# Kernel optimization log

Measured on AMD Instinct MI355X. Metric: run time of the kernel, lower is better.

## Reference

```python
import jax, jax.numpy as jnp
import numpy as np

B, C, E, H = 8, 2048, 1024, 128


def setup_inputs() -> dict:
    key = jax.random.key(0)
    k1, k2, k3, k4 = jax.random.split(key, 4)
    x = jax.random.normal(k1, (B, C, E), dtype=jnp.float32)
    # store projection weights as (E, H) so projection is x @ W
    Wq = jax.random.normal(k2, (E, H), dtype=jnp.float32) * (E ** -0.5)
    Wk = jax.random.normal(k3, (E, H), dtype=jnp.float32) * (E ** -0.5)
    Wv = jax.random.normal(k4, (E, H), dtype=jnp.float32) * (E ** -0.5)
    return {"x": x, "Wq": Wq, "Wk": Wk, "Wv": Wv}


def reference(x, Wq, Wk, Wv):
    # x: (B, C, E) -> out: (B, C, H)
    _, c, e = x.shape
    q = x @ Wq  # (B, C, H)
    k = x @ Wk  # (B, C, H)
    v = x @ Wv  # (B, C, H)
    # NOTE: original scales by embed_size**0.5, not head_size**0.5
    scale = jnp.asarray(e, x.dtype) ** 0.5
    w = jnp.einsum('bqh,bkh->bqk', q, k) / scale  # (B, C, C)
    causal = jnp.tril(jnp.ones((c, c), dtype=bool))
    w = jnp.where(causal, w, -jnp.inf)
    w = jax.nn.softmax(w, axis=-1)
    # dropout_rate = 0.0 -> identity (eval mode)
    out = w @ v  # (B, C, H)
    return out
```

## Files before the change

kernel.cpp:

```cpp
#include <hip/hip_runtime.h>
#include <hip/hip_bf16.h>
#include <stdint.h>

#define B_ 8
#define C_ 2048
#define E_ 1024
#define H_ 128
#define M_ (B_*C_)
#define SLOTS_B 144

typedef __attribute__((ext_vector_type(8))) short bf16x8;
typedef __attribute__((ext_vector_type(4))) float f32x4;

__device__ __forceinline__ unsigned short f2bf(float f) {
    union { float f; unsigned int u; } v; v.f = f;
    unsigned int u = v.u;
    u += 0x7fff + ((u >> 16) & 1);
    return (unsigned short)(u >> 16);
}
__device__ __forceinline__ float bf2f(unsigned short u) {
    union { unsigned int i; float f; } v; v.i = ((unsigned int)u) << 16; return v.f;
}

#define GLOAD_LDS16(g, l) \
    __builtin_amdgcn_global_load_lds((const __attribute__((address_space(1))) void*)(g), \
                                     (__attribute__((address_space(3))) void*)(l), 16, 0, 0)

__global__ __launch_bounds__(256) void wt2_kernel(const float* __restrict__ Wq,
                                                  const float* __restrict__ Wk,
                                                  const float* __restrict__ Wv,
                                                  unsigned short* __restrict__ WT2) {
    int z = blockIdx.y;
    const float* W = (z == 0) ? Wq : (z == 1) ? Wk : Wv;
    unsigned short* o = WT2 + (size_t)z * H_ * E_;
    int gid = blockIdx.x * 256 + threadIdx.x;
    int g = gid >> 7, h = gid & 127;
    unsigned short t[8];
#pragma unroll
    for (int j = 0; j < 8; ++j)
        t[j] = f2bf(W[(size_t)(g * 8 + j) * H_ + h]);
    *(bf16x8*)&o[(size_t)(g * 128 + h) * 8] = *(const bf16x8*)t;
}

#define MF(a, b, c) __builtin_amdgcn_mfma_f32_16x16x32_bf16((a), (b), (c), 0, 0, 0)

#define ALOAD(S, T) { const float* xs_ = xrow + (T) * 64; \
    a##S##_0 = *(const float4*)xs_;        a##S##_1 = *(const float4*)(xs_ + 4); \
    a##S##_2 = *(const float4*)(xs_ + 8);  a##S##_3 = *(const float4*)(xs_ + 12); }

#define AWRITE(S, BUF) { \
    unsigned short t0_[8] = {f2bf(a##S##_0.x), f2bf(a##S##_0.y), f2bf(a##S##_0.z), f2bf(a##S##_0.w), \
                             f2bf(a##S##_1.x), f2bf(a##S##_1.y), f2bf(a##S##_1.z), f2bf(a##S##_1.w)}; \
    unsigned short t1_[8] = {f2bf(a##S##_2.x), f2bf(a##S##_2.y), f2bf(a##S##_2.z), f2bf(a##S##_2.w), \
                             f2bf(a##S##_3.x), f2bf(a##S##_3.y), f2bf(a##S##_3.z), f2bf(a##S##_3.w)}; \
    *(bf16x8*)&As[BUF][arow][(ag0 ^ (arow & 7)) * 8]       = *(const bf16x8*)t0_; \
    *(bf16x8*)&As[BUF][arow][((ag0 + 1) ^ (arow & 7)) * 8] = *(const bf16x8*)t1_; }

#define BLOAD(S, T) { const unsigned short* wp_ = wbase + (size_t)(T) * 8192; \
    b##S##0 = *(const bf16x8*)(wp_);        b##S##1 = *(const bf16x8*)(wp_ + 128); \
    b##S##2 = *(const bf16x8*)(wp_ + 256);  b##S##3 = *(const bf16x8*)(wp_ + 384); \
    b##S##4 = *(const bf16x8*)(wp_ + 4096); b##S##5 = *(const bf16x8*)(wp_ + 4224); \
    b##S##6 = *(const bf16x8*)(wp_ + 4352); b##S##7 = *(const bf16x8*)(wp_ + 4480); }

#define COMPUTE(BUF, S) { \
    bf16x8 af00 = *(const bf16x8*)&As[BUF][ra0][(lq ^ (ra0 & 7)) * 8]; \
    bf16x8 af01 = *(const bf16x8*)&As[BUF][ra1][(lq ^ (ra1 & 7)) * 8]; \
    acc[0][0] = MF(af00, b##S##0, acc[0][0]);  acc[1][0] = MF(af01, b##S##0, acc[1][0]); \
    acc[0][1] = MF(af00, b##S##1, acc[0][1]);  acc[1][1] = MF(af01, b##S##1, acc[1][1]); \
    acc[0][2] = MF(af00, b##S##2, acc[0][2]);  acc[1][2] = MF(af01, b##S##2, acc[1][2]); \
    acc[0][3] = MF(af00, b##S##3, acc[0][3]);  acc[1][3] = MF(af01, b##S##3, acc[1][3]); \
    bf16x8 af10 = *(const bf16x8*)&As[BUF][ra0][((4 + lq) ^ (ra0 & 7)) * 8]; \
    bf16x8 af11 = *(const bf16x8*)&As[BUF][ra1][((4 + lq) ^ (ra1 & 7)) * 8]; \
    acc[0][0] = MF(af10, b##S##4, acc[0][0]);  acc[1][0] = MF(af11, b##S##4, acc[1][0]); \
    acc[0][1] = MF(af10, b##S##5, acc[0][1]);  acc[1][1] = MF(af11, b##S##5, acc[1][1]); \
    acc[0][2] = MF(af10, b##S##6, acc[0][2]);  acc[1][2] = MF(af11, b##S##6, acc[1][2]); \
    acc[0][3] = MF(af10, b##S##7, acc[0][3]);  acc[1][3] = MF(af11, b##S##7, acc[1][3]); }

#define EVEN_STEP(K) { \
    __syncthreads(); \
    AWRITE(B, 1);                                   \
    if ((K) + 3 <= 15) ALOAD(B, (K) + 3); \
    COMPUTE(0, A);                                  \
    if ((K) + 2 <= 15) BLOAD(A, (K) + 2); }

#define ODD_STEP(K) { \
    __syncthreads(); \
    if ((K) + 1 <= 15) AWRITE(A, 0);                \
    if ((K) + 3 <= 15) ALOAD(A, (K) + 3); \
    COMPUTE(1, B);                                  \
    if ((K) + 2 <= 15) BLOAD(B, (K) + 2); }

__global__ __launch_bounds__(256) void proj_kernel(const float* __restrict__ x,
                                                   const unsigned short* __restrict__ WT2,
                                                   unsigned short* __restrict__ QKV) {
    __shared__ __align__(16) unsigned short As[2][64][64];

    const int tid = threadIdx.x;
    const int wid = tid >> 6, lane = tid & 63;
    const int lrow = lane & 15, lq = lane >> 4;
    const int wr = wid >> 1, wc = wid & 1;
    const int row0 = blockIdx.x * 64;
    const int w = blockIdx.y;
    const unsigned short* wt = WT2 + (size_t)w * H_ * E_;

    const int arow = tid >> 2;
    const int ag0 = (tid & 3) * 2;
    const float* xrow = x + (size_t)(row0 + arow) * E_ + ag0 * 8;
    const int ra0 = wr * 32 + lrow, ra1 = wr * 32 + 16 + lrow;

    const unsigned short* wbase = wt + (size_t)(lq * 128 + wc * 64 + lrow) * 8;

    f32x4 acc[2][4];
#pragma unroll
    for (int mi = 0; mi < 2; ++mi)
#pragma unroll
        for (int ni = 0; ni < 4; ++ni) acc[mi][ni] = (f32x4){0.f, 0.f, 0.f, 0.f};

    float4 aA_0, aA_1, aA_2, aA_3, aB_0, aB_1, aB_2, aB_3;
    bf16x8 bA0, bA1, bA2, bA3, bA4, bA5, bA6, bA7;
    bf16x8 bB0, bB1, bB2, bB3, bB4, bB5, bB6, bB7;

    ALOAD(A, 0); BLOAD(A, 0);
    ALOAD(B, 1); BLOAD(B, 1);
    AWRITE(A, 0);
    ALOAD(A, 2);

    EVEN_STEP(0)  ODD_STEP(1)  EVEN_STEP(2)  ODD_STEP(3)
    EVEN_STEP(4)  ODD_STEP(5)  EVEN_STEP(6)  ODD_STEP(7)
    EVEN_STEP(8)  ODD_STEP(9)  EVEN_STEP(10) ODD_STEP(11)
    EVEN_STEP(12) ODD_STEP(13) EVEN_STEP(14) ODD_STEP(15)

    if (w < 2) {
        const float qs = (w == 0) ? 0.03125f : 1.0f;
        unsigned short* outp = QKV + (size_t)w * M_ * H_;
#pragma unroll
        for (int mi = 0; mi < 2; ++mi) {
            int r0 = row0 + wr * 32 + mi * 16 + lq * 4;
#pragma unroll
            for (int ni = 0; ni < 4; ++ni) {
                int col = wc * 64 + ni * 16 + lrow;
#pragma unroll
                for (int r = 0; r < 4; ++r)
                    outp[(size_t)(r0 + r) * H_ + col] = f2bf(acc[mi][ni][r] * qs);
            }
        }
    } else {
        unsigned short* vt = QKV + (size_t)2 * M_ * H_;
        int b = row0 / C_;
        int cbase = row0 % C_;
#pragma unroll
        for (int mi = 0; mi < 2; ++mi) {
            int c0 = cbase + wr * 32 + mi * 16 + lq * 4;
#pragma unroll
            for (int ni = 0; ni < 4; ++ni) {
                int h = wc * 64 + ni * 16 + lrow;
                __align__(8) unsigned short p[4] = {f2bf(acc[mi][ni][0]), f2bf(acc[mi][ni][1]),
                                                    f2bf(acc[mi][ni][2]), f2bf(acc[mi][ni][3])};
                *(uint2*)&vt[((size_t)b * H_ + h) * C_ + c0] = *(const uint2*)p;
            }
        }
    }
}

__global__ __launch_bounds__(256) void attn_kernel(const unsigned short* __restrict__ QKV,
                                                   unsigned short* __restrict__ PO,
                                                   float* __restrict__ ML,
                                                   float* __restrict__ out) {
    __shared__ __align__(16) unsigned short Ks[2][64][128];
    __shared__ __align__(16) unsigned short Vt[2][128][64];
    __shared__ __align__(16) unsigned short Ps[4][16][72];

    const unsigned short* Q  = QKV;
    const unsigned short* K  = QKV + (size_t)M_ * H_;
    const unsigned short* VT = QKV + (size_t)2 * M_ * H_;

    const int tid = threadIdx.x, wid = tid >> 6, lane = tid & 63;
    const int lrow = lane & 15, lq = lane >> 4, lk = lq * 8;
    const int rr = blockIdx.x;
    const int b = blockIdx.y;

    int j = 0;
#pragma unroll
    for (int jj = 1; jj < 32; ++jj) {
        int q = jj >> 2, s = jj & 3;
        if (jj + 2 * q * (q - 1) + s * q <= rr) j = jj;
    }
    const int qj = j >> 2, sj = j & 3;
    const int Cj = j + 2 * qj * (qj - 1) + sj * qj;
    const int c = rr - Cj;
    const int nch = qj + 1;
    const int t0 = c * 4;
    const int t1 = min(t0 + 4, j + 1);

    const int q0w = j * 64 + wid * 16;
    const unsigned short* Kb  = K  + (size_t)b * C_ * H_;
    const unsigned short* VTb = VT + (size_t)b * H_ * C_;
    const int qrow0 = q0w + lq * 4;

    const int krow = tid >> 4, kg = tid & 15;
    const int vrow = tid >> 3, vg = tid & 7;

    bf16x8 qf[4];
#pragma unroll
    for (int kf = 0; kf < 4; ++kf)
        qf[kf] = *(const bf16x8*)&Q[((size_t)b * C_ + q0w + lrow) * H_ + kf * 32 + lk];

    f32x4 o[8];
#pragma unroll
    for (int nf = 0; nf < 8; ++nf) o[nf] = (f32x4){0.f, 0.f, 0.f, 0.f};
    float m[4] = {-INFINITY, -INFINITY, -INFINITY, -INFINITY};
    float l[4] = {0.f, 0.f, 0.f, 0.f};

    auto STAGE = [&](int buf, int t) {
        const int kv0 = t * 64;
#pragma unroll
        for (int s = 0; s < 4; ++s) {
            int r = s * 16 + krow;
            GLOAD_LDS16(&Kb[(size_t)(kv0 + r) * H_ + ((kg ^ (r & 15)) * 8)],
                        (char*)&Ks[buf][0][0] + s * 4096 + tid * 16);
        }
#pragma unroll
        for (int s = 0; s < 4; ++s) {
            int h = s * 32 + vrow;
            GLOAD_LDS16(&VTb[(size_t)h * C_ + kv0 + ((vg ^ (h & 7)) * 8)],
                        (char*)&Vt[buf][0][0] + s * 4096 + tid * 16);
        }
    };

    STAGE(0, t0);

    for (int t = t0; t < t1; ++t) {
        const int cur = (t - t0) & 1;
        __syncthreads();
        if (t + 1 < t1) STAGE(cur ^ 1, t + 1);

        const int kv0 = t * 64;
        f32x4 s[4];
#pragma unroll
        for (int nf = 0; nf < 4; ++nf) {
            s[nf] = (f32x4){0.f, 0.f, 0.f, 0.f};
            const int rk = nf * 16 + lrow;
#pragma unroll
            for (int kf = 0; kf < 4; ++kf) {
                bf16x8 kb = *(const bf16x8*)&Ks[cur][rk][((kf * 4 + lq) ^ (rk & 15)) * 8];
                s[nf] = __builtin_amdgcn_mfma_f32_16x16x32_bf16(qf[kf], kb, s[nf], 0, 0, 0);
            }
        }
        bf16x8 vb[8][2];
#pragma unroll
        for (int nf = 0; nf < 8; ++nf) {
            const int h = nf * 16 + lrow;
#pragma unroll
            for (int kf2 = 0; kf2 < 2; ++kf2)
                vb[nf][kf2] = *(const bf16x8*)&Vt[cur][h][((kf2 * 4 + lq) ^ (h & 7)) * 8];
        }

        if (t == j) {
#pragma unroll
            for (int nf = 0; nf < 4; ++nf) {
                int key = kv0 + nf * 16 + lrow;
#pragma unroll
                for (int r = 0; r < 4; ++r)
                    if (key > qrow0 + r) s[nf][r] = -INFINITY;
            }
        }
        float mt[4] = {-INFINITY, -INFINITY, -INFINITY, -INFINITY};
#pragma unroll
        for (int nf = 0; nf < 4; ++nf)
#pragma unroll
            for (int r = 0; r < 4; ++r) mt[r] = fmaxf(mt[r], s[nf][r]);
#pragma unroll
        for (int r = 0; r < 4; ++r)
#pragma unroll
            for (int off = 1; off < 16; off <<= 1)
                mt[r] = fmaxf(mt[r], __shfl_xor(mt[r], off));

        float corr[4];
#pragma unroll
        for (int r = 0; r < 4; ++r) {
            float mn = fmaxf(m[r], mt[r]);
            corr[r] = __expf(m[r] - mn);
            m[r] = mn;
        }
        float ps[4] = {0.f, 0.f, 0.f, 0.f};
#pragma unroll
        for (int nf = 0; nf < 4; ++nf)
#pragma unroll
            for (int r = 0; r < 4; ++r) {
                float p = __expf(s[nf][r] - m[r]);
                ps[r] += p;
                Ps[wid][lq * 4 + r][nf * 16 + lrow] = f2bf(p);
            }
#pragma unroll
        for (int r = 0; r < 4; ++r) {
#pragma unroll
            for (int off = 1; off < 16; off <<= 1) ps[r] += __shfl_xor(ps[r], off);
            l[r] = l[r] * corr[r] + ps[r];
        }
#pragma unroll
        for (int nf = 0; nf < 8; ++nf)
#pragma unroll
            for (int r = 0; r < 4; ++r) o[nf][r] *= corr[r];

        bf16x8 pa[2];
#pragma unroll
        for (int kf2 = 0; kf2 < 2; ++kf2)
            pa[kf2] = *(const bf16x8*)&Ps[wid][lrow][kf2 * 32 + lk];
#pragma unroll
        for (int nf = 0; nf < 8; ++nf)
#pragma unroll
            for (int kf2 = 0; kf2 < 2; ++kf2)
                o[nf] = __builtin_amdgcn_mfma_f32_16x16x32_bf16(pa[kf2], vb[nf][kf2], o[nf], 0, 0, 0);
    }

    if (nch == 1) {
#pragma unroll
        for (int nf = 0; nf < 8; ++nf) {
            int col = nf * 16 + lrow;
#pragma unroll
            for (int r = 0; r < 4; ++r)
                out[((size_t)b * C_ + qrow0 + r) * H_ + col] = o[nf][r] / l[r];
        }
    } else {
        const int slot = b * SLOTS_B + rr;
        unsigned short* po = PO + (size_t)slot * 64 * 128;
        const int rl0 = wid * 16 + lq * 4;
#pragma unroll
        for (int nf = 0; nf < 8; ++nf) {
            int col = nf * 16 + lrow;
#pragma unroll
            for (int r = 0; r < 4; ++r)
                po[(size_t)(rl0 + r) * 128 + col] = f2bf(o[nf][r]);
        }
        if (lrow == 0) {
            float* ml = ML + (size_t)slot * 128;
#pragma unroll
            for (int r = 0; r < 4; ++r) {
                ml[rl0 + r] = m[r];
                ml[64 + rl0 + r] = l[r];
            }
        }
    }
}

__global__ __launch_bounds__(256) void combine_kernel(const unsigned short* __restrict__ PO,
                                                      const float* __restrict__ ML,
                                                      float* __restrict__ out) {
    const int j = blockIdx.x + 4;
    const int b = blockIdx.y;
    const int q = j >> 2, s = j & 3;
    const int Cj = j + 2 * q * (q - 1) + s * q;
    const int nch = q + 1;
    const int base = b * SLOTS_B + Cj;
    const int row = threadIdx.x >> 2;
    const int colg = (threadIdx.x & 3) * 32;

    float mstar = -INFINITY;
    for (int c = 0; c < nch; ++c)
        mstar = fmaxf(mstar, ML[(size_t)(base + c) * 128 + row]);

    float denom = 0.f;
    float acc[32];
#pragma unroll
    for (int i = 0; i < 32; ++i) acc[i] = 0.f;

    for (int c = 0; c < nch; ++c) {
        float mc = ML[(size_t)(base + c) * 128 + row];
        float lc = ML[(size_t)(base + c) * 128 + 64 + row];
        float w = __expf(mc - mstar);
        denom += w * lc;
        const unsigned short* p = PO + (size_t)(base + c) * 64 * 128 + (size_t)row * 128 + colg;
#pragma unroll
        for (int k = 0; k < 4; ++k) {
            bf16x8 v = *(const bf16x8*)&p[k * 8];
#pragma unroll
            for (int e = 0; e < 8; ++e)
                acc[k * 8 + e] += w * bf2f(((unsigned short*)&v)[e]);
        }
    }
    float inv = 1.f / denom;
    float* op = out + ((size_t)b * C_ + j * 64 + row) * H_ + colg;
#pragma unroll
    for (int k = 0; k < 8; ++k) {
        float4 st = {acc[k * 4] * inv, acc[k * 4 + 1] * inv, acc[k * 4 + 2] * inv, acc[k * 4 + 3] * inv};
        *(float4*)&op[k * 4] = st;
    }
}

extern "C" void kernel_launch(void* const* d_in, const int* in_sizes, int n_in,
                              void* d_out, int out_size, void* d_ws, size_t ws_size,
                              hipStream_t stream) {
    const float* x  = (const float*)d_in[0];
    const float* Wq = (const float*)d_in[1];
    const float* Wk = (const float*)d_in[2];
    const float* Wv = (const float*)d_in[3];
    float* out = (float*)d_out;

    unsigned short* WT2 = (unsigned short*)d_ws;
    unsigned short* QKV = WT2 + (size_t)3 * H_ * E_;
    unsigned short* PO  = QKV + (size_t)3 * M_ * H_;
    float*          ML  = (float*)(PO + (size_t)8 * SLOTS_B * 64 * 128);

    wt2_kernel<<<dim3(E_ / 8 * H_ / 256, 3), 256, 0, stream>>>(Wq, Wk, Wv, WT2);
    proj_kernel<<<dim3(M_ / 64, 3), 256, 0, stream>>>(x, WT2, QKV);
    attn_kernel<<<dim3(SLOTS_B, B_), 256, 0, stream>>>(QKV, PO, ML, out);
    combine_kernel<<<dim3(28, B_), 256, 0, stream>>>(PO, ML, out);
}
```

Before: 83.96 us.

## Fuse Q/K/V projections into one block per 32-row x tile

Each projection block now computes all three Q, K and V outputs for a 32-row tile of x instead of one weight matrix per 64-row tile. This means x is read from HBM and converted to bf16 once rather than three times. The B-operand register prefetch pipeline is removed, and weight fragments are loaded directly from global memory inside each step. That risks exposed global-load latency, and the three accumulator sets raise register pressure.

```diff
diff --git a/kernel.cpp b/kernel.cpp
--- a/kernel.cpp
+++ b/kernel.cpp
@@ -45,117 +45,106 @@
 #define MF(a, b, c) __builtin_amdgcn_mfma_f32_16x16x32_bf16((a), (b), (c), 0, 0, 0)
 
 #define ALOAD(S, T) { const float* xs_ = xrow + (T) * 64; \
-    a##S##_0 = *(const float4*)xs_;        a##S##_1 = *(const float4*)(xs_ + 4); \
-    a##S##_2 = *(const float4*)(xs_ + 8);  a##S##_3 = *(const float4*)(xs_ + 12); }
+    a##S##_0 = *(const float4*)xs_;  a##S##_1 = *(const float4*)(xs_ + 4); }
 
 #define AWRITE(S, BUF) { \
-    unsigned short t0_[8] = {f2bf(a##S##_0.x), f2bf(a##S##_0.y), f2bf(a##S##_0.z), f2bf(a##S##_0.w), \
-                             f2bf(a##S##_1.x), f2bf(a##S##_1.y), f2bf(a##S##_1.z), f2bf(a##S##_1.w)}; \
-    unsigned short t1_[8] = {f2bf(a##S##_2.x), f2bf(a##S##_2.y), f2bf(a##S##_2.z), f2bf(a##S##_2.w), \
-                             f2bf(a##S##_3.x), f2bf(a##S##_3.y), f2bf(a##S##_3.z), f2bf(a##S##_3.w)}; \
-    *(bf16x8*)&As[BUF][arow][(ag0 ^ (arow & 7)) * 8]       = *(const bf16x8*)t0_; \
-    *(bf16x8*)&As[BUF][arow][((ag0 + 1) ^ (arow & 7)) * 8] = *(const bf16x8*)t1_; }
-
-#define BLOAD(S, T) { const unsigned short* wp_ = wbase + (size_t)(T) * 8192; \
-    b##S##0 = *(const bf16x8*)(wp_);        b##S##1 = *(const bf16x8*)(wp_ + 128); \
-    b##S##2 = *(const bf16x8*)(wp_ + 256);  b##S##3 = *(const bf16x8*)(wp_ + 384); \
-    b##S##4 = *(const bf16x8*)(wp_ + 4096); b##S##5 = *(const bf16x8*)(wp_ + 4224); \
-    b##S##6 = *(const bf16x8*)(wp_ + 4352); b##S##7 = *(const bf16x8*)(wp_ + 4480); }
-
-#define COMPUTE(BUF, S) { \
-    bf16x8 af00 = *(const bf16x8*)&As[BUF][ra0][(lq ^ (ra0 & 7)) * 8]; \
-    bf16x8 af01 = *(const bf16x8*)&As[BUF][ra1][(lq ^ (ra1 & 7)) * 8]; \
-    acc[0][0] = MF(af00, b##S##0, acc[0][0]);  acc[1][0] = MF(af01, b##S##0, acc[1][0]); \
-    acc[0][1] = MF(af00, b##S##1, acc[0][1]);  acc[1][1] = MF(af01, b##S##1, acc[1][1]); \
-    acc[0][2] = MF(af00, b##S##2, acc[0][2]);  acc[1][2] = MF(af01, b##S##2, acc[1][2]); \
-    acc[0][3] = MF(af00, b##S##3, acc[0][3]);  acc[1][3] = MF(af01, b##S##3, acc[1][3]); \
-    bf16x8 af10 = *(const bf16x8*)&As[BUF][ra0][((4 + lq) ^ (ra0 & 7)) * 8]; \
-    bf16x8 af11 = *(const bf16x8*)&As[BUF][ra1][((4 + lq) ^ (ra1 & 7)) * 8]; \
-    acc[0][0] = MF(af10, b##S##4, acc[0][0]);  acc[1][0] = MF(af11, b##S##4, acc[1][0]); \
-    acc[0][1] = MF(af10, b##S##5, acc[0][1]);  acc[1][1] = MF(af11, b##S##5, acc[1][1]); \
-    acc[0][2] = MF(af10, b##S##6, acc[0][2]);  acc[1][2] = MF(af11, b##S##6, acc[1][2]); \
-    acc[0][3] = MF(af10, b##S##7, acc[0][3]);  acc[1][3] = MF(af11, b##S##7, acc[1][3]); }
+    unsigned short t_[8] = {f2bf(a##S##_0.x), f2bf(a##S##_0.y), f2bf(a##S##_0.z), f2bf(a##S##_0.w), \
+                            f2bf(a##S##_1.x), f2bf(a##S##_1.y), f2bf(a##S##_1.z), f2bf(a##S##_1.w)}; \
+    *(bf16x8*)&As[BUF][arow][(ag ^ (arow & 7)) * 8] = *(const bf16x8*)t_; }
+
+#define COMPUTE(BUF, T) { \
+    bf16x8 bw[3][2][2]; \
+    _Pragma("unroll") for (int w_ = 0; w_ < 3; ++w_) \
+    _Pragma("unroll") for (int ks_ = 0; ks_ < 2; ++ks_) \
+    _Pragma("unroll") for (int ni_ = 0; ni_ < 2; ++ni_) \
+        bw[w_][ni_][ks_] = *(const bf16x8*)&WT2[(size_t)w_ * H_ * E_ + \
+            (size_t)(((T) * 8 + ks_ * 4 + lq) * 128 + wcol + ni_ * 16 + lrow) * 8]; \
+    bf16x8 af[2][2]; \
+    _Pragma("unroll") for (int mi_ = 0; mi_ < 2; ++mi_) \
+    _Pragma("unroll") for (int ks_ = 0; ks_ < 2; ++ks_) { \
+        int ra_ = mi_ * 16 + lrow; \
+        af[mi_][ks_] = *(const bf16x8*)&As[BUF][ra_][((ks_ * 4 + lq) ^ (ra_ & 7)) * 8]; \
+    } \
+    _Pragma("unroll") for (int ks_ = 0; ks_ < 2; ++ks_) \
+    _Pragma("unroll") for (int w_ = 0; w_ < 3; ++w_) \
+    _Pragma("unroll") for (int ni_ = 0; ni_ < 2; ++ni_) \
+    _Pragma("unroll") for (int mi_ = 0; mi_ < 2; ++mi_) \
+        acc[w_][mi_][ni_] = MF(af[mi_][ks_], bw[w_][ni_][ks_], acc[w_][mi_][ni_]); }
 
 #define EVEN_STEP(K) { \
     __syncthreads(); \
-    AWRITE(B, 1);                                   \
-    if ((K) + 3 <= 15) ALOAD(B, (K) + 3); \
-    COMPUTE(0, A);                                  \
-    if ((K) + 2 <= 15) BLOAD(A, (K) + 2); }
+    if ((K) + 1 <= 15) AWRITE(B, 1);                \
+    if ((K) + 2 <= 15) ALOAD(A, (K) + 2); \
+    COMPUTE(0, K); }
 
 #define ODD_STEP(K) { \
     __syncthreads(); \
     if ((K) + 1 <= 15) AWRITE(A, 0);                \
-    if ((K) + 3 <= 15) ALOAD(A, (K) + 3); \
-    COMPUTE(1, B);                                  \
-    if ((K) + 2 <= 15) BLOAD(B, (K) + 2); }
+    if ((K) + 2 <= 15) ALOAD(B, (K) + 2); \
+    COMPUTE(1, K); }
 
 __global__ __launch_bounds__(256) void proj_kernel(const float* __restrict__ x,
                                                    const unsigned short* __restrict__ WT2,
                                                    unsigned short* __restrict__ QKV) {
-    __shared__ __align__(16) unsigned short As[2][64][64];
+    __shared__ __align__(16) unsigned short As[2][32][64];
 
     const int tid = threadIdx.x;
     const int wid = tid >> 6, lane = tid & 63;
     const int lrow = lane & 15, lq = lane >> 4;
-    const int wr = wid >> 1, wc = wid & 1;
-    const int row0 = blockIdx.x * 64;
-    const int w = blockIdx.y;
-    const unsigned short* wt = WT2 + (size_t)w * H_ * E_;
-
-    const int arow = tid >> 2;
-    const int ag0 = (tid & 3) * 2;
-    const float* xrow = x + (size_t)(row0 + arow) * E_ + ag0 * 8;
-    const int ra0 = wr * 32 + lrow, ra1 = wr * 32 + 16 + lrow;
-
-    const unsigned short* wbase = wt + (size_t)(lq * 128 + wc * 64 + lrow) * 8;
-
-    f32x4 acc[2][4];
-#pragma unroll
-    for (int mi = 0; mi < 2; ++mi)
-#pragma unroll
-        for (int ni = 0; ni < 4; ++ni) acc[mi][ni] = (f32x4){0.f, 0.f, 0.f, 0.f};
-
-    float4 aA_0, aA_1, aA_2, aA_3, aB_0, aB_1, aB_2, aB_3;
-    bf16x8 bA0, bA1, bA2, bA3, bA4, bA5, bA6, bA7;
-    bf16x8 bB0, bB1, bB2, bB3, bB4, bB5, bB6, bB7;
-
-    ALOAD(A, 0); BLOAD(A, 0);
-    ALOAD(B, 1); BLOAD(B, 1);
+    const int wcol = wid * 32;
+    const int row0 = blockIdx.x * 32;
+
+    const int arow = tid >> 3;
+    const int ag = tid & 7;
+    const float* xrow = x + (size_t)(row0 + arow) * E_ + ag * 8;
+
+    f32x4 acc[3][2][2];
+#pragma unroll
+    for (int w = 0; w < 3; ++w)
+#pragma unroll
+        for (int mi = 0; mi < 2; ++mi)
+#pragma unroll
+            for (int ni = 0; ni < 2; ++ni) acc[w][mi][ni] = (f32x4){0.f, 0.f, 0.f, 0.f};
+
+    float4 aA_0, aA_1, aB_0, aB_1;
+
+    ALOAD(A, 0);
     AWRITE(A, 0);
-    ALOAD(A, 2);
+    ALOAD(B, 1);
 
     EVEN_STEP(0)  ODD_STEP(1)  EVEN_STEP(2)  ODD_STEP(3)
     EVEN_STEP(4)  ODD_STEP(5)  EVEN_STEP(6)  ODD_STEP(7)
     EVEN_STEP(8)  ODD_STEP(9)  EVEN_STEP(10) ODD_STEP(11)
     EVEN_STEP(12) ODD_STEP(13) EVEN_STEP(14) ODD_STEP(15)
 
-    if (w < 2) {
+#pragma unroll
+    for (int w = 0; w < 2; ++w) {
         const float qs = (w == 0) ? 0.03125f : 1.0f;
         unsigned short* outp = QKV + (size_t)w * M_ * H_;
 #pragma unroll
         for (int mi = 0; mi < 2; ++mi) {
-            int r0 = row0 + wr * 32 + mi * 16 + lq * 4;
-#pragma unroll
-            for (int ni = 0; ni < 4; ++ni) {
-                int col = wc * 64 + ni * 16 + lrow;
+            int r0 = row0 + mi * 16 + lq * 4;
+#pragma unroll
+            for (int ni = 0; ni < 2; ++ni) {
+                int col = wcol + ni * 16 + lrow;
 #pragma unroll
                 for (int r = 0; r < 4; ++r)
-                    outp[(size_t)(r0 + r) * H_ + col] = f2bf(acc[mi][ni][r] * qs);
-            }
-        }
-    } else {
+                    outp[(size_t)(r0 + r) * H_ + col] = f2bf(acc[w][mi][ni][r] * qs);
+            }
+        }
+    }
+    {
         unsigned short* vt = QKV + (size_t)2 * M_ * H_;
         int b = row0 / C_;
         int cbase = row0 % C_;
 #pragma unroll
         for (int mi = 0; mi < 2; ++mi) {
-            int c0 = cbase + wr * 32 + mi * 16 + lq * 4;
-#pragma unroll
-            for (int ni = 0; ni < 4; ++ni) {
-                int h = wc * 64 + ni * 16 + lrow;
-                __align__(8) unsigned short p[4] = {f2bf(acc[mi][ni][0]), f2bf(acc[mi][ni][1]),
-                                                    f2bf(acc[mi][ni][2]), f2bf(acc[mi][ni][3])};
+            int c0 = cbase + mi * 16 + lq * 4;
+#pragma unroll
+            for (int ni = 0; ni < 2; ++ni) {
+                int h = wcol + ni * 16 + lrow;
+                __align__(8) unsigned short p[4] = {f2bf(acc[2][mi][ni][0]), f2bf(acc[2][mi][ni][1]),
+                                                    f2bf(acc[2][mi][ni][2]), f2bf(acc[2][mi][ni][3])};
                 *(uint2*)&vt[((size_t)b * H_ + h) * C_ + c0] = *(const uint2*)p;
             }
         }
@@ -402,7 +391,7 @@
     float*          ML  = (float*)(PO + (size_t)8 * SLOTS_B * 64 * 128);
 
     wt2_kernel<<<dim3(E_ / 8 * H_ / 256, 3), 256, 0, stream>>>(Wq, Wk, Wv, WT2);
-    proj_kernel<<<dim3(M_ / 64, 3), 256, 0, stream>>>(x, WT2, QKV);
+    proj_kernel<<<dim3(M_ / 32), 256, 0, stream>>>(x, WT2, QKV);
     attn_kernel<<<dim3(SLOTS_B, B_), 256, 0, stream>>>(QKV, PO, ML, out);
     combine_kernel<<<dim3(28, B_), 256, 0, stream>>>(PO, ML, out);
 }
```

After: 79.46 us. 1.06x faster.
